# Kernel optimization log

Hardware: AMD Instinct MI355X
Metric: run time of the kernel (lower is better)

Reference implementation:

```python
import jax, jax.numpy as jnp
import numpy as np

D = 131072  # inner feature dim
N = 84      # 4*(1 + 4*(1 + 4)) entries emitted by calc_probs


def calc_probs(logits):
    # softmax over the 4 logits, then emit, in original nested-loop order:
    # for i: p_i, then for j: p_i*p_j followed by p_i*p_j*p_k for k in 0..3
    p = jax.nn.softmax(logits)                      # (4,)
    pairs = p[:, None] * p[None, :]                 # (4,4)
    triples = pairs[:, :, None] * p[None, None, :]  # (4,4,4)
    inner = jnp.concatenate([pairs[:, :, None], triples], axis=2)  # (4,4,5)
    full = jnp.concatenate([p[:, None], inner.reshape(4, 20)], axis=1)  # (4,21)
    return full.reshape(N)  # (84,)


def setup_inputs() -> dict:
    key = jax.random.key(0)
    ks = jax.random.split(key, 6)
    return {
        "BEV": jax.random.normal(ks[0], (1,), dtype=jnp.float32),
        "ST0": jax.random.normal(ks[1], (N, D), dtype=jnp.float32),
        "Weight0": jax.random.normal(ks[2], (N, D, 1), dtype=jnp.float32),
        "ST1": jax.random.normal(ks[3], (N, D), dtype=jnp.float32),
        "Weight1": jax.random.normal(ks[4], (N, D, 1), dtype=jnp.float32),
        "Problem": 1,
        "probs0": jnp.array([2.0327, 1.0198, 1.024, 0.9935], dtype=jnp.float32),
        "probs1": jnp.array([2.6661, 1.0168, 1.02, 0.9971], dtype=jnp.float32),
        "probs2": jnp.array([2.8173, 1.016, 1.0189, 0.9978], dtype=jnp.float32),
        "probs3": jnp.array([2.9183, 1.0154, 1.0181, 0.9981], dtype=jnp.float32),
        "probs4": jnp.array([2.9689, 1.0151, 1.0177, 0.9983], dtype=jnp.float32),
        "pBEV": jnp.array([0.1822], dtype=jnp.float32),
        "pB": jnp.array([3.1475], dtype=jnp.float32),
    }


def reference(BEV, ST0, Weight0, ST1, Weight1, Problem,
              probs0, probs1, probs2, probs3, probs4, pBEV, pB):
    p0 = calc_probs(probs0)
    p1 = calc_probs(probs1)
    p2 = calc_probs(probs2)
    p3 = calc_probs(probs3)
    p4 = calc_probs(probs4)
    # fused sigmoid + per-row dot, replacing the Python loop over 84 rows
    bev = pBEV * BEV  # (1,)
    tmp0 = jnp.einsum('id,id->i', jax.nn.sigmoid(pB * (bev + ST0)), Weight0[..., 0])  # (84,)
    tmp1 = jnp.einsum('id,id->i', jax.nn.sigmoid(pB * (bev + ST1)), Weight1[..., 0])  # (84,)
    vals = jnp.stack([p0 @ tmp0, p1 @ tmp1, p2 @ tmp1, p3 @ tmp1, p4 @ tmp1])
    return jnp.mean(vals)
```

## Files before the change

kernel.cpp:

```cpp
#include <hip/hip_runtime.h>
#include <hip/hip_bf16.h>


#define D_DIM         131072
#define N_ROWS        84
#define ROW_F4        (D_DIM / 4)
#define TENSOR_F4     (N_ROWS * ROW_F4)
#define F4_PER_BLOCK  1024
#define T0_BLOCKS     (TENSOR_F4 / F4_PER_BLOCK)
#define BLOCKS        (2 * T0_BLOCKS)

typedef float f32x4 __attribute__((ext_vector_type(4)));

__device__ inline float prob_entry(const float* __restrict__ logits, int t) {
    float l0 = logits[0], l1 = logits[1], l2 = logits[2], l3 = logits[3];
    float m  = fmaxf(fmaxf(l0, l1), fmaxf(l2, l3));
    float e0 = __expf(l0 - m), e1 = __expf(l1 - m);
    float e2 = __expf(l2 - m), e3 = __expf(l3 - m);
    float inv = 1.0f / (e0 + e1 + e2 + e3);
    float p[4] = {e0 * inv, e1 * inv, e2 * inv, e3 * inv};
    int i = t / 21;
    int r = t - i * 21;
    if (r == 0) return p[i];
    r -= 1;
    int j = r / 5;
    int s = r - j * 5;
    float v = p[i] * p[j];
    return (s == 0) ? v : v * p[s - 1];
}

__device__ inline float sigdot(float w, float s, float a, float ab) {
    float e = __builtin_amdgcn_exp2f(fmaf(a, s, ab));
    return w * __builtin_amdgcn_rcpf(1.0f + e);
}

__global__ __launch_bounds__(256, 4) void probsnet_main(
    const float* __restrict__ BEV,
    const float* __restrict__ ST0, const float* __restrict__ W0,
    const float* __restrict__ ST1, const float* __restrict__ W1,
    const float* __restrict__ probs0, const float* __restrict__ probs1,
    const float* __restrict__ probs2, const float* __restrict__ probs3,
    const float* __restrict__ probs4,
    const float* __restrict__ pBEV, const float* __restrict__ pB,
    float* __restrict__ partials)
{
    const int bid    = blockIdx.x;
    const int t      = threadIdx.x;
    const int tensor = (bid >= T0_BLOCKS) ? 1 : 0;
    const int fb     = (bid - tensor * T0_BLOCKS) * F4_PER_BLOCK;
    const int row    = fb >> 15;

    const float pb  = pB[0];
    const float bev = pBEV[0] * BEV[0];
    const float a   = -pb * 1.4426950408889634f;
    const float ab  = a * bev;

    const f32x4* sp = (const f32x4*)(tensor ? ST1 : ST0) + fb + t;
    const f32x4* wp = (const f32x4*)(tensor ? W1  : W0 ) + fb + t;

    f32x4 s0, s1, s2, s3, w0, w1, w2, w3;
    asm volatile(
        "global_load_dwordx4 %0, %8, off\n\t"
        "global_load_dwordx4 %4, %12, off\n\t"
        "global_load_dwordx4 %1, %9, off\n\t"
        "global_load_dwordx4 %5, %13, off\n\t"
        "global_load_dwordx4 %2, %10, off\n\t"
        "global_load_dwordx4 %6, %14, off\n\t"
        "global_load_dwordx4 %3, %11, off\n\t"
        "global_load_dwordx4 %7, %15, off\n\t"
        "s_waitcnt vmcnt(0)"
        : "=&v"(s0), "=&v"(s1), "=&v"(s2), "=&v"(s3),
          "=&v"(w0), "=&v"(w1), "=&v"(w2), "=&v"(w3)
        : "v"(sp), "v"(sp + 256), "v"(sp + 512), "v"(sp + 768),
          "v"(wp), "v"(wp + 256), "v"(wp + 512), "v"(wp + 768));

    float acc = 0.0f;
    acc += sigdot(w0[0], s0[0], a, ab); acc += sigdot(w0[1], s0[1], a, ab);
    acc += sigdot(w0[2], s0[2], a, ab); acc += sigdot(w0[3], s0[3], a, ab);
    acc += sigdot(w1[0], s1[0], a, ab); acc += sigdot(w1[1], s1[1], a, ab);
    acc += sigdot(w1[2], s1[2], a, ab); acc += sigdot(w1[3], s1[3], a, ab);
    acc += sigdot(w2[0], s2[0], a, ab); acc += sigdot(w2[1], s2[1], a, ab);
    acc += sigdot(w2[2], s2[2], a, ab); acc += sigdot(w2[3], s2[3], a, ab);
    acc += sigdot(w3[0], s3[0], a, ab); acc += sigdot(w3[1], s3[1], a, ab);
    acc += sigdot(w3[2], s3[2], a, ab); acc += sigdot(w3[3], s3[3], a, ab);

    #pragma unroll
    for (int off = 32; off > 0; off >>= 1)
        acc += __shfl_down(acc, off, 64);

    __shared__ float red[4];
    const int wave = t >> 6;
    const int lane = t & 63;
    if (lane == 0) red[wave] = acc;
    __syncthreads();

    if (t == 0) {
        const float S = red[0] + red[1] + red[2] + red[3];
        float pw;
        if (tensor == 0) {
            pw = prob_entry(probs0, row);
        } else {
            pw = prob_entry(probs1, row) + prob_entry(probs2, row)
               + prob_entry(probs3, row) + prob_entry(probs4, row);
        }
        partials[bid] = pw * S;
    }
}

__global__ __launch_bounds__(256) void probsnet_reduce(
    const float* __restrict__ partials, float* __restrict__ out)
{
    const int t = threadIdx.x;
    float acc = 0.0f;
    #pragma unroll
    for (int k = 0; k < BLOCKS / 256; ++k)
        acc += partials[t + k * 256];

    #pragma unroll
    for (int off = 32; off > 0; off >>= 1)
        acc += __shfl_down(acc, off, 64);

    __shared__ float red[4];
    const int wave = t >> 6;
    const int lane = t & 63;
    if (lane == 0) red[wave] = acc;
    __syncthreads();

    if (t == 0)
        out[0] = (red[0] + red[1] + red[2] + red[3]) * 0.2f;
}

extern "C" void kernel_launch(void* const* d_in, const int* in_sizes, int n_in,
                              void* d_out, int out_size, void* d_ws, size_t ws_size,
                              hipStream_t stream) {
    const float* BEV    = (const float*)d_in[0];
    const float* ST0    = (const float*)d_in[1];
    const float* W0     = (const float*)d_in[2];
    const float* ST1    = (const float*)d_in[3];
    const float* W1     = (const float*)d_in[4];
    const float* probs0 = (const float*)d_in[6];
    const float* probs1 = (const float*)d_in[7];
    const float* probs2 = (const float*)d_in[8];
    const float* probs3 = (const float*)d_in[9];
    const float* probs4 = (const float*)d_in[10];
    const float* pBEV   = (const float*)d_in[11];
    const float* pB     = (const float*)d_in[12];

    float* partials = (float*)d_ws;
    float* out      = (float*)d_out;

    probsnet_main<<<BLOCKS, 256, 0, stream>>>(
        BEV, ST0, W0, ST1, W1,
        probs0, probs1, probs2, probs3, probs4,
        pBEV, pB, partials);

    probsnet_reduce<<<1, 256, 0, stream>>>(partials, out);
}
```

Baseline: 201.2 us.

## Process four chunks per block with double-buffered inline-asm global loads

Each block now covers four 1024-float4 chunks instead of one, cutting the main grid to a quarter of its previous size. Two register sets alternate: the next chunk's loads are issued before the current chunk's sigmoid-dot work, with partial vmcnt waits so loads overlap arithmetic and more bytes stay in flight per wave. Loads switch to SGPR-base plus 32-bit VGPR-offset addressing, which saves address registers. The reduce kernel becomes a strided loop sized for the smaller partials array. The trade-off is higher register pressure and fewer blocks to spread across CUs.

```diff
diff --git a/kernel.cpp b/kernel.cpp
--- a/kernel.cpp
+++ b/kernel.cpp
@@ -1,14 +1,15 @@
 #include <hip/hip_runtime.h>
-#include <hip/hip_bf16.h>
-
-
-#define D_DIM         131072
-#define N_ROWS        84
-#define ROW_F4        (D_DIM / 4)
-#define TENSOR_F4     (N_ROWS * ROW_F4)
-#define F4_PER_BLOCK  1024
-#define T0_BLOCKS     (TENSOR_F4 / F4_PER_BLOCK)
-#define BLOCKS        (2 * T0_BLOCKS)
+
+
+#define D_DIM          131072
+#define N_ROWS         84
+#define ROW_F4         (D_DIM / 4)
+#define F4_PER_CHUNK   1024
+#define CHUNK_BYTES    (F4_PER_CHUNK * 16)
+#define CPB            4
+#define BLOCKS_PER_ROW (ROW_F4 / (F4_PER_CHUNK * CPB))
+#define T0_BLOCKS      (N_ROWS * BLOCKS_PER_ROW)
+#define BLOCKS         (2 * T0_BLOCKS)
 
 typedef float f32x4 __attribute__((ext_vector_type(4)));
 
@@ -34,6 +35,51 @@
     return w * __builtin_amdgcn_rcpf(1.0f + e);
 }
 
+#define ISSUE8(S0, S1, S2, S3, Wa, Wb_, Wc, Wd, off, SB, WB)               \
+    asm volatile(                                                          \
+        "global_load_dwordx4 %0, %8, %12\n\t"                              \
+        "global_load_dwordx4 %4, %8, %13\n\t"                              \
+        "global_load_dwordx4 %1, %9, %12\n\t"                              \
+        "global_load_dwordx4 %5, %9, %13\n\t"                              \
+        "global_load_dwordx4 %2, %10, %12\n\t"                             \
+        "global_load_dwordx4 %6, %10, %13\n\t"                             \
+        "global_load_dwordx4 %3, %11, %12\n\t"                             \
+        "global_load_dwordx4 %7, %11, %13"                                 \
+        : "=&v"(S0), "=&v"(S1), "=&v"(S2), "=&v"(S3),                      \
+          "=&v"(Wa), "=&v"(Wb_), "=&v"(Wc), "=&v"(Wd)                      \
+        : "v"(off), "v"((off) + 4096u), "v"((off) + 8192u),                \
+          "v"((off) + 12288u), "s"(SB), "s"(WB))
+
+#define WAIT_PREV8(S0, S1, S2, S3, Wa, Wb_, Wc, Wd)                        \
+    asm volatile("s_waitcnt vmcnt(8)"                                      \
+                 : "+v"(S0), "+v"(S1), "+v"(S2), "+v"(S3),                 \
+                   "+v"(Wa), "+v"(Wb_), "+v"(Wc), "+v"(Wd))
+
+#define WAIT_ALL8(S0, S1, S2, S3, Wa, Wb_, Wc, Wd)                         \
+    asm volatile("s_waitcnt vmcnt(0)"                                      \
+                 : "+v"(S0), "+v"(S1), "+v"(S2), "+v"(S3),                 \
+                   "+v"(Wa), "+v"(Wb_), "+v"(Wc), "+v"(Wd))
+
+#define ACC16(S0, S1, S2, S3, Wa, Wb_, Wc, Wd)                             \
+    do {                                                                   \
+        acc += sigdot(Wa[0], S0[0], a, ab);                                \
+        acc += sigdot(Wa[1], S0[1], a, ab);                                \
+        acc += sigdot(Wa[2], S0[2], a, ab);                                \
+        acc += sigdot(Wa[3], S0[3], a, ab);                                \
+        acc += sigdot(Wb_[0], S1[0], a, ab);                               \
+        acc += sigdot(Wb_[1], S1[1], a, ab);                               \
+        acc += sigdot(Wb_[2], S1[2], a, ab);                               \
+        acc += sigdot(Wb_[3], S1[3], a, ab);                               \
+        acc += sigdot(Wc[0], S2[0], a, ab);                                \
+        acc += sigdot(Wc[1], S2[1], a, ab);                                \
+        acc += sigdot(Wc[2], S2[2], a, ab);                                \
+        acc += sigdot(Wc[3], S2[3], a, ab);                                \
+        acc += sigdot(Wd[0], S3[0], a, ab);                                \
+        acc += sigdot(Wd[1], S3[1], a, ab);                                \
+        acc += sigdot(Wd[2], S3[2], a, ab);                                \
+        acc += sigdot(Wd[3], S3[3], a, ab);                                \
+    } while (0)
+
 __global__ __launch_bounds__(256, 4) void probsnet_main(
     const float* __restrict__ BEV,
     const float* __restrict__ ST0, const float* __restrict__ W0,
@@ -47,42 +93,40 @@
     const int bid    = blockIdx.x;
     const int t      = threadIdx.x;
     const int tensor = (bid >= T0_BLOCKS) ? 1 : 0;
-    const int fb     = (bid - tensor * T0_BLOCKS) * F4_PER_BLOCK;
-    const int row    = fb >> 15;
+    const int cb     = bid - tensor * T0_BLOCKS;
+    const int row    = cb / BLOCKS_PER_ROW;
 
     const float pb  = pB[0];
     const float bev = pBEV[0] * BEV[0];
     const float a   = -pb * 1.4426950408889634f;
     const float ab  = a * bev;
 
-    const f32x4* sp = (const f32x4*)(tensor ? ST1 : ST0) + fb + t;
-    const f32x4* wp = (const f32x4*)(tensor ? W1  : W0 ) + fb + t;
-
-    f32x4 s0, s1, s2, s3, w0, w1, w2, w3;
-    asm volatile(
-        "global_load_dwordx4 %0, %8, off\n\t"
-        "global_load_dwordx4 %4, %12, off\n\t"
-        "global_load_dwordx4 %1, %9, off\n\t"
-        "global_load_dwordx4 %5, %13, off\n\t"
-        "global_load_dwordx4 %2, %10, off\n\t"
-        "global_load_dwordx4 %6, %14, off\n\t"
-        "global_load_dwordx4 %3, %11, off\n\t"
-        "global_load_dwordx4 %7, %15, off\n\t"
-        "s_waitcnt vmcnt(0)"
-        : "=&v"(s0), "=&v"(s1), "=&v"(s2), "=&v"(s3),
-          "=&v"(w0), "=&v"(w1), "=&v"(w2), "=&v"(w3)
-        : "v"(sp), "v"(sp + 256), "v"(sp + 512), "v"(sp + 768),
-          "v"(wp), "v"(wp + 256), "v"(wp + 512), "v"(wp + 768));
+    const float* Sb = tensor ? ST1 : ST0;
+    const float* Wb = tensor ? W1  : W0;
+
+    const unsigned base = (unsigned)(cb * (CPB * F4_PER_CHUNK) + t) * 16u;
+
+    f32x4 as0, as1, as2, as3, aw0, aw1, aw2, aw3;
+    f32x4 bs0, bs1, bs2, bs3, bw0, bw1, bw2, bw3;
 
     float acc = 0.0f;
-    acc += sigdot(w0[0], s0[0], a, ab); acc += sigdot(w0[1], s0[1], a, ab);
-    acc += sigdot(w0[2], s0[2], a, ab); acc += sigdot(w0[3], s0[3], a, ab);
-    acc += sigdot(w1[0], s1[0], a, ab); acc += sigdot(w1[1], s1[1], a, ab);
-    acc += sigdot(w1[2], s1[2], a, ab); acc += sigdot(w1[3], s1[3], a, ab);
-    acc += sigdot(w2[0], s2[0], a, ab); acc += sigdot(w2[1], s2[1], a, ab);
-    acc += sigdot(w2[2], s2[2], a, ab); acc += sigdot(w2[3], s2[3], a, ab);
-    acc += sigdot(w3[0], s3[0], a, ab); acc += sigdot(w3[1], s3[1], a, ab);
-    acc += sigdot(w3[2], s3[2], a, ab); acc += sigdot(w3[3], s3[3], a, ab);
+
+    ISSUE8(as0, as1, as2, as3, aw0, aw1, aw2, aw3, base,                   Sb, Wb);
+    ISSUE8(bs0, bs1, bs2, bs3, bw0, bw1, bw2, bw3, base + 1u * CHUNK_BYTES, Sb, Wb);
+
+    WAIT_PREV8(as0, as1, as2, as3, aw0, aw1, aw2, aw3);
+    ACC16(as0, as1, as2, as3, aw0, aw1, aw2, aw3);
+    ISSUE8(as0, as1, as2, as3, aw0, aw1, aw2, aw3, base + 2u * CHUNK_BYTES, Sb, Wb);
+
+    WAIT_PREV8(bs0, bs1, bs2, bs3, bw0, bw1, bw2, bw3);
+    ACC16(bs0, bs1, bs2, bs3, bw0, bw1, bw2, bw3);
+    ISSUE8(bs0, bs1, bs2, bs3, bw0, bw1, bw2, bw3, base + 3u * CHUNK_BYTES, Sb, Wb);
+
+    WAIT_PREV8(as0, as1, as2, as3, aw0, aw1, aw2, aw3);
+    ACC16(as0, as1, as2, as3, aw0, aw1, aw2, aw3);
+
+    WAIT_ALL8(bs0, bs1, bs2, bs3, bw0, bw1, bw2, bw3);
+    ACC16(bs0, bs1, bs2, bs3, bw0, bw1, bw2, bw3);
 
     #pragma unroll
     for (int off = 32; off > 0; off >>= 1)
@@ -112,9 +156,8 @@
 {
     const int t = threadIdx.x;
     float acc = 0.0f;
-    #pragma unroll
-    for (int k = 0; k < BLOCKS / 256; ++k)
-        acc += partials[t + k * 256];
+    for (int k = t; k < BLOCKS; k += 256)
+        acc += partials[k];
 
     #pragma unroll
     for (int off = 32; off > 0; off >>= 1)
```

Result: no change. 203.7 us (+1.3%).

## Use persistent 256-block grid with software-pipelined double-buffered loads

Applied to the files above, without the earlier changes.

Replaces the one-shot grid of 5376 blocks, each loading 16 KB and waiting on all loads, with 256 persistent blocks. Each block walks 21 tasks of 16 KB using two register buffer sets and partial vmcnt waits, so loads for upcoming tasks stay in flight while the current one is computed. The probability weights are applied per task inside the loop, and the reduce kernel now sums only 256 partials. The aim is to hide memory latency and cut block-launch overhead, but with one block per CU there is less occupancy available to cover stalls. Correctness also depends on the hand-written waitcnt counts.

```diff
diff --git a/kernel.cpp b/kernel.cpp
--- a/kernel.cpp
+++ b/kernel.cpp
@@ -1,14 +1,11 @@
 #include <hip/hip_runtime.h>
-#include <hip/hip_bf16.h>
-
-
-#define D_DIM         131072
-#define N_ROWS        84
-#define ROW_F4        (D_DIM / 4)
-#define TENSOR_F4     (N_ROWS * ROW_F4)
-#define F4_PER_BLOCK  1024
-#define T0_BLOCKS     (TENSOR_F4 / F4_PER_BLOCK)
-#define BLOCKS        (2 * T0_BLOCKS)
+
+
+#define D_DIM           131072
+#define N_ROWS          84
+#define TASKS_PER_BLOCK 21
+#define BLOCKS          256
+#define TASK_BYTES      16384
 
 typedef float f32x4 __attribute__((ext_vector_type(4)));
 
@@ -34,7 +31,44 @@
     return w * __builtin_amdgcn_rcpf(1.0f + e);
 }
 
-__global__ __launch_bounds__(256, 4) void probsnet_main(
+#define ISSUE(SX, WX, OFFC)                                                \
+    asm volatile("global_load_dwordx4 %0, %4, %2\n\t"                      \
+                 "global_load_dwordx4 %1, %4, %3"                          \
+                 : "=&v"(SX), "=&v"(WX)                                    \
+                 : "s"(Sb), "s"(Wb), "v"(vbase + (unsigned)(OFFC)))
+
+#define WAITP(N, SX, WX)                                                   \
+    asm volatile("s_waitcnt vmcnt(%2)"                                     \
+                 : "+v"(SX), "+v"(WX) : "n"(N))
+
+#define ACC8(SX, WX)                                                       \
+    do {                                                                   \
+        acc_t += sigdot(WX[0], SX[0], a, ab);                              \
+        acc_t += sigdot(WX[1], SX[1], a, ab);                              \
+        acc_t += sigdot(WX[2], SX[2], a, ab);                              \
+        acc_t += sigdot(WX[3], SX[3], a, ab);                              \
+    } while (0)
+
+#define STEP(SX, WX, N, ISS, OFFC)                                         \
+    do {                                                                   \
+        WAITP(N, SX, WX);                                                  \
+        ACC8(SX, WX);                                                      \
+        if (ISS) { ISSUE(SX, WX, OFFC); }                                  \
+    } while (0)
+
+#define TASK(J, A0,B0,A1,B1,A2,B2,A3,B3, N0,N1,N2,N3, ISS)                 \
+    do {                                                                   \
+        const int   row_ = (tb21 + (J)) >> 5;                              \
+        const float pw_  = (row_ == r0) ? pw0 : pw1;                       \
+        float acc_t = 0.0f;                                                \
+        STEP(A0, B0, N0, ISS, ((J) + 2) * TASK_BYTES + 0 * 1024);          \
+        STEP(A1, B1, N1, ISS, ((J) + 2) * TASK_BYTES + 1 * 1024);          \
+        STEP(A2, B2, N2, ISS, ((J) + 2) * TASK_BYTES + 2 * 1024);          \
+        STEP(A3, B3, N3, ISS, ((J) + 2) * TASK_BYTES + 3 * 1024);          \
+        acc = fmaf(pw_, acc_t, acc);                                       \
+    } while (0)
+
+__global__ __launch_bounds__(256, 1) void probsnet_main(
     const float* __restrict__ BEV,
     const float* __restrict__ ST0, const float* __restrict__ W0,
     const float* __restrict__ ST1, const float* __restrict__ W1,
@@ -44,77 +78,91 @@
     const float* __restrict__ pBEV, const float* __restrict__ pB,
     float* __restrict__ partials)
 {
-    const int bid    = blockIdx.x;
+    const int b      = blockIdx.x;
     const int t      = threadIdx.x;
-    const int tensor = (bid >= T0_BLOCKS) ? 1 : 0;
-    const int fb     = (bid - tensor * T0_BLOCKS) * F4_PER_BLOCK;
-    const int row    = fb >> 15;
+    const int tensor = b >> 7;
+    const int tb     = b & 127;
+    const int tb21   = tb * TASKS_PER_BLOCK;
+    const int wv     = t >> 6;
+    const int lane   = t & 63;
 
     const float pb  = pB[0];
     const float bev = pBEV[0] * BEV[0];
     const float a   = -pb * 1.4426950408889634f;
     const float ab  = a * bev;
 
-    const f32x4* sp = (const f32x4*)(tensor ? ST1 : ST0) + fb + t;
-    const f32x4* wp = (const f32x4*)(tensor ? W1  : W0 ) + fb + t;
-
-    f32x4 s0, s1, s2, s3, w0, w1, w2, w3;
-    asm volatile(
-        "global_load_dwordx4 %0, %8, off\n\t"
-        "global_load_dwordx4 %4, %12, off\n\t"
-        "global_load_dwordx4 %1, %9, off\n\t"
-        "global_load_dwordx4 %5, %13, off\n\t"
-        "global_load_dwordx4 %2, %10, off\n\t"
-        "global_load_dwordx4 %6, %14, off\n\t"
-        "global_load_dwordx4 %3, %11, off\n\t"
-        "global_load_dwordx4 %7, %15, off\n\t"
-        "s_waitcnt vmcnt(0)"
-        : "=&v"(s0), "=&v"(s1), "=&v"(s2), "=&v"(s3),
-          "=&v"(w0), "=&v"(w1), "=&v"(w2), "=&v"(w3)
-        : "v"(sp), "v"(sp + 256), "v"(sp + 512), "v"(sp + 768),
-          "v"(wp), "v"(wp + 256), "v"(wp + 512), "v"(wp + 768));
+    const float* Sb = tensor ? ST1 : ST0;
+    const float* Wb = tensor ? W1  : W0;
+
+    const int r0 = tb21 >> 5;
+    const int r1 = (tb21 + TASKS_PER_BLOCK - 1) >> 5;
+    float pw0, pw1;
+    if (tensor == 0) {
+        pw0 = prob_entry(probs0, r0);
+        pw1 = prob_entry(probs0, r1);
+    } else {
+        pw0 = prob_entry(probs1, r0) + prob_entry(probs2, r0)
+            + prob_entry(probs3, r0) + prob_entry(probs4, r0);
+        pw1 = prob_entry(probs1, r1) + prob_entry(probs2, r1)
+            + prob_entry(probs3, r1) + prob_entry(probs4, r1);
+    }
+
+    const unsigned vbase = (unsigned)tb21 * TASK_BYTES
+                         + (unsigned)wv * 4096u + (unsigned)lane * 16u;
+
+    f32x4 vs0, vs1, vs2, vs3, vs4, vs5, vs6, vs7;
+    f32x4 vw0, vw1, vw2, vw3, vw4, vw5, vw6, vw7;
 
     float acc = 0.0f;
-    acc += sigdot(w0[0], s0[0], a, ab); acc += sigdot(w0[1], s0[1], a, ab);
-    acc += sigdot(w0[2], s0[2], a, ab); acc += sigdot(w0[3], s0[3], a, ab);
-    acc += sigdot(w1[0], s1[0], a, ab); acc += sigdot(w1[1], s1[1], a, ab);
-    acc += sigdot(w1[2], s1[2], a, ab); acc += sigdot(w1[3], s1[3], a, ab);
-    acc += sigdot(w2[0], s2[0], a, ab); acc += sigdot(w2[1], s2[1], a, ab);
-    acc += sigdot(w2[2], s2[2], a, ab); acc += sigdot(w2[3], s2[3], a, ab);
-    acc += sigdot(w3[0], s3[0], a, ab); acc += sigdot(w3[1], s3[1], a, ab);
-    acc += sigdot(w3[2], s3[2], a, ab); acc += sigdot(w3[3], s3[3], a, ab);
+
+    ISSUE(vs0, vw0, 0 * TASK_BYTES + 0 * 1024);
+    ISSUE(vs1, vw1, 0 * TASK_BYTES + 1 * 1024);
+    ISSUE(vs2, vw2, 0 * TASK_BYTES + 2 * 1024);
+    ISSUE(vs3, vw3, 0 * TASK_BYTES + 3 * 1024);
+    ISSUE(vs4, vw4, 1 * TASK_BYTES + 0 * 1024);
+    ISSUE(vs5, vw5, 1 * TASK_BYTES + 1 * 1024);
+    ISSUE(vs6, vw6, 1 * TASK_BYTES + 2 * 1024);
+    ISSUE(vs7, vw7, 1 * TASK_BYTES + 3 * 1024);
+
+    TASK( 0, vs0,vw0,vs1,vw1,vs2,vw2,vs3,vw3, 14,14,14,14, 1);
+    TASK( 1, vs4,vw4,vs5,vw5,vs6,vw6,vs7,vw7, 14,14,14,14, 1);
+    TASK( 2, vs0,vw0,vs1,vw1,vs2,vw2,vs3,vw3, 14,14,14,14, 1);
+    TASK( 3, vs4,vw4,vs5,vw5,vs6,vw6,vs7,vw7, 14,14,14,14, 1);
+    TASK( 4, vs0,vw0,vs1,vw1,vs2,vw2,vs3,vw3, 14,14,14,14, 1);
+    TASK( 5, vs4,vw4,vs5,vw5,vs6,vw6,vs7,vw7, 14,14,14,14, 1);
+    TASK( 6, vs0,vw0,vs1,vw1,vs2,vw2,vs3,vw3, 14,14,14,14, 1);
+    TASK( 7, vs4,vw4,vs5,vw5,vs6,vw6,vs7,vw7, 14,14,14,14, 1);
+    TASK( 8, vs0,vw0,vs1,vw1,vs2,vw2,vs3,vw3, 14,14,14,14, 1);
+    TASK( 9, vs4,vw4,vs5,vw5,vs6,vw6,vs7,vw7, 14,14,14,14, 1);
+    TASK(10, vs0,vw0,vs1,vw1,vs2,vw2,vs3,vw3, 14,14,14,14, 1);
+    TASK(11, vs4,vw4,vs5,vw5,vs6,vw6,vs7,vw7, 14,14,14,14, 1);
+    TASK(12, vs0,vw0,vs1,vw1,vs2,vw2,vs3,vw3, 14,14,14,14, 1);
+    TASK(13, vs4,vw4,vs5,vw5,vs6,vw6,vs7,vw7, 14,14,14,14, 1);
+    TASK(14, vs0,vw0,vs1,vw1,vs2,vw2,vs3,vw3, 14,14,14,14, 1);
+    TASK(15, vs4,vw4,vs5,vw5,vs6,vw6,vs7,vw7, 14,14,14,14, 1);
+    TASK(16, vs0,vw0,vs1,vw1,vs2,vw2,vs3,vw3, 14,14,14,14, 1);
+    TASK(17, vs4,vw4,vs5,vw5,vs6,vw6,vs7,vw7, 14,14,14,14, 1);
+    TASK(18, vs0,vw0,vs1,vw1,vs2,vw2,vs3,vw3, 14,14,14,14, 1);
+    TASK(19, vs4,vw4,vs5,vw5,vs6,vw6,vs7,vw7, 14,12,10, 8, 0);
+    TASK(20, vs0,vw0,vs1,vw1,vs2,vw2,vs3,vw3,  6, 4, 2, 0, 0);
 
     #pragma unroll
     for (int off = 32; off > 0; off >>= 1)
         acc += __shfl_down(acc, off, 64);
 
     __shared__ float red[4];
-    const int wave = t >> 6;
-    const int lane = t & 63;
-    if (lane == 0) red[wave] = acc;
+    if (lane == 0) red[wv] = acc;
     __syncthreads();
 
-    if (t == 0) {
-        const float S = red[0] + red[1] + red[2] + red[3];
-        float pw;
-        if (tensor == 0) {
-            pw = prob_entry(probs0, row);
-        } else {
-            pw = prob_entry(probs1, row) + prob_entry(probs2, row)
-               + prob_entry(probs3, row) + prob_entry(probs4, row);
-        }
-        partials[bid] = pw * S;
-    }
+    if (t == 0)
+        partials[b] = red[0] + red[1] + red[2] + red[3];
 }
 
 __global__ __launch_bounds__(256) void probsnet_reduce(
     const float* __restrict__ partials, float* __restrict__ out)
 {
     const int t = threadIdx.x;
-    float acc = 0.0f;
-    #pragma unroll
-    for (int k = 0; k < BLOCKS / 256; ++k)
-        acc += partials[t + k * 256];
+    float acc = partials[t];
 
     #pragma unroll
     for (int off = 32; off > 0; off >>= 1)
```

Result: slower. 206.5 us (+2.6%).
